# Kernel tuning notes

Hardware: AMD Instinct MI355X
Metric: run time of the kernel (lower is better)

The kernel has to match this reference:

```python
import jax, jax.numpy as jnp
import numpy as np

N_HEAD = 16


def setup_inputs() -> dict:
    key = jax.random.key(0)
    k0, k1, k2, k3 = jax.random.split(key, 4)
    b, n, d = 4, 2048, 1024
    scale = d ** -0.5
    return {
        "x": jax.random.normal(k0, (b, n, d), jnp.float32),
        "Wk": jax.random.normal(k1, (d, d), jnp.float32) * scale,
        "Wq": jax.random.normal(k2, (d, d), jnp.float32) * scale,
        "Wv": jax.random.normal(k3, (d, d), jnp.float32) * scale,
    }


def reference(x, Wk, Wq, Wv):
    b, n, d = x.shape
    hd = d // N_HEAD
    # Linear layers: y = x @ W^T (torch nn.Linear convention), no bias.
    keys = (x @ Wk.T).reshape(b, n, N_HEAD, hd).transpose(0, 2, 1, 3)     # (b,h,n,hd)
    queries = (x @ Wq.T).reshape(b, n, N_HEAD, hd).transpose(0, 2, 1, 3)  # (b,h,n,hd)
    values = (x @ Wv.T).reshape(b, n, N_HEAD, hd).transpose(0, 2, 1, 3)   # computed but UNUSED, as in source
    del values
    # Source does: attn_scores = keys @ queries.transpose(-1,-2)
    # i.e. scores[b,h,i,j] = k_i . q_j ; softmax over j (query axis); no 1/sqrt(d) scaling.
    attn_scores = jnp.einsum("bhid,bhjd->bhij", keys, queries)
    weights = jax.nn.softmax(attn_scores, axis=-1)
    # Source does: weight_scores @ keys (keys, NOT values)
    weighted = jnp.einsum("bhij,bhjd->bhid", weights, keys)  # (b,h,n,hd)
    # Source reshapes (b,h,n,hd) directly to (b,n,h*hd) WITHOUT transposing back.
    return weighted.reshape(b, n, N_HEAD * hd)
```

## Files before the change

### kernel.cpp

```cpp
#include <hip/hip_runtime.h>
#include <cstdint>
#include <cstddef>

#define NTOK 2048
#define DMODEL 1024
#define HD 64
#define MROWS 8192

using f16x8  = __attribute__((ext_vector_type(8))) _Float16;
using f16x4  = __attribute__((ext_vector_type(4))) _Float16;
using f32x4  = __attribute__((ext_vector_type(4))) float;
using f32x16 = __attribute__((ext_vector_type(16))) float;
using u16x8  = __attribute__((ext_vector_type(8))) unsigned short;
using u32x4  = __attribute__((ext_vector_type(4))) unsigned int;

#define Z16 {0.f,0.f,0.f,0.f,0.f,0.f,0.f,0.f,0.f,0.f,0.f,0.f,0.f,0.f,0.f,0.f}

__device__ __forceinline__ unsigned pkf16(float a, float b) {
  return __builtin_bit_cast(unsigned, __builtin_amdgcn_cvt_pkrtz(a, b));
}
__device__ __forceinline__ void plswap(unsigned &a, unsigned &b) {
  auto r = __builtin_amdgcn_permlane32_swap(a, b, false, false);
  a = r[0]; b = r[1];
}
__device__ __forceinline__ float fexp2(float x) {
  return __builtin_amdgcn_exp2f(x);
}

__global__ __launch_bounds__(256) void cvt_f32_f16(const float* __restrict__ in,
                                                   _Float16* __restrict__ out,
                                                   int n4, float scale) {
  int idx = blockIdx.x * 256 + threadIdx.x;
  if (idx < n4) {
    float4 v = reinterpret_cast<const float4*>(in)[idx];
    f16x4 o;
    o.x = (_Float16)(v.x * scale); o.y = (_Float16)(v.y * scale);
    o.z = (_Float16)(v.z * scale); o.w = (_Float16)(v.w * scale);
    reinterpret_cast<f16x4*>(out)[idx] = o;
  }
}

__global__ __launch_bounds__(256) void cvt_w(const float* __restrict__ Wk,
                                             const float* __restrict__ Wq,
                                             _Float16* __restrict__ Wkb,
                                             _Float16* __restrict__ Wqb) {
  const int idx = blockIdx.x * 256 + threadIdx.x;
  const float* in = blockIdx.y ? Wq : Wk;
  _Float16* out = blockIdx.y ? Wqb : Wkb;
  const float scale = blockIdx.y ? 1.4426950408889634f : 1.0f;
  float4 v = reinterpret_cast<const float4*>(in)[idx];
  f16x4 o;
  o.x = (_Float16)(v.x * scale); o.y = (_Float16)(v.y * scale);
  o.z = (_Float16)(v.z * scale); o.w = (_Float16)(v.w * scale);
  reinterpret_cast<f16x4*>(out)[idx] = o;
}

#define GLDS16(g, l) __builtin_amdgcn_global_load_lds(                      \
    (const __attribute__((address_space(1))) void*)(g),                     \
    (__attribute__((address_space(3))) void*)(l), 16, 0, 0)

__global__ __launch_bounds__(256) void gemm_f16(
    const _Float16* __restrict__ X,
    const _Float16* __restrict__ Wk,
    const _Float16* __restrict__ Wq,
    _Float16* __restrict__ Kb,
    _Float16* __restrict__ Qb) {
  const _Float16* __restrict__ W = blockIdx.z ? Wq : Wk;
  _Float16* __restrict__ Y = blockIdx.z ? Qb : Kb;

  __shared__ _Float16 As[2][128 * 32];
  __shared__ _Float16 Bs[2][128 * 32];

  const int tid = threadIdx.x;
  const int lane = tid & 63;
  const int w = tid >> 6;
  const int m0 = blockIdx.x * 128;
  const int o0 = blockIdx.y * 128;

  const int srow = w * 32 + (lane >> 2);
  const int scol = (lane & 3) * 8;
  const _Float16* xsrc = X + (size_t)(m0 + srow) * DMODEL + scol;
  const _Float16* wsrc = W + (size_t)(o0 + srow) * DMODEL + scol;

  const int wr = w >> 1, wc = w & 1;
  const int arow = lane & 15, kg = lane >> 4;

  f32x4 zero = {0.f, 0.f, 0.f, 0.f};
  f32x4 acc[4][4];
#pragma unroll
  for (int mi = 0; mi < 4; ++mi)
#pragma unroll
    for (int ni = 0; ni < 4; ++ni) acc[mi][ni] = zero;

  GLDS16(xsrc,               &As[0][(w * 32) * 32]);
  GLDS16(xsrc + 16 * DMODEL, &As[0][(w * 32 + 16) * 32]);
  GLDS16(wsrc,               &Bs[0][(w * 32) * 32]);
  GLDS16(wsrc + 16 * DMODEL, &Bs[0][(w * 32 + 16) * 32]);

  for (int kt = 0; kt < 32; ++kt) {
    __syncthreads();
    if (kt + 1 < 32) {
      const int ko = (kt + 1) * 32;
      const int bn = (kt + 1) & 1;
      GLDS16(xsrc + ko,               &As[bn][(w * 32) * 32]);
      GLDS16(xsrc + ko + 16 * DMODEL, &As[bn][(w * 32 + 16) * 32]);
      GLDS16(wsrc + ko,               &Bs[bn][(w * 32) * 32]);
      GLDS16(wsrc + ko + 16 * DMODEL, &Bs[bn][(w * 32 + 16) * 32]);
    }
    const int buf = kt & 1;
    f16x8 af[4], bfr[4];
#pragma unroll
    for (int mi = 0; mi < 4; ++mi)
      af[mi] = *reinterpret_cast<const f16x8*>(
          &As[buf][(wr * 64 + mi * 16 + arow) * 32 + kg * 8]);
#pragma unroll
    for (int ni = 0; ni < 4; ++ni)
      bfr[ni] = *reinterpret_cast<const f16x8*>(
          &Bs[buf][(wc * 64 + ni * 16 + arow) * 32 + kg * 8]);
#pragma unroll
    for (int mi = 0; mi < 4; ++mi)
#pragma unroll
      for (int ni = 0; ni < 4; ++ni)
        acc[mi][ni] = __builtin_amdgcn_mfma_f32_16x16x32_f16(
            af[mi], bfr[ni], acc[mi][ni], 0, 0, 0);
  }

#pragma unroll
  for (int mi = 0; mi < 4; ++mi) {
#pragma unroll
    for (int ni = 0; ni < 4; ++ni) {
#pragma unroll
      for (int r = 0; r < 4; ++r) {
        const int m = m0 + wr * 64 + mi * 16 + kg * 4 + r;
        const int o = o0 + wc * 64 + ni * 16 + arow;
        Y[(size_t)m * DMODEL + o] = (_Float16)acc[mi][ni][r];
      }
    }
  }
}

__global__ __launch_bounds__(256) void pack_qkt(
    const _Float16* __restrict__ Qb,
    const _Float16* __restrict__ Kb,
    _Float16* __restrict__ Qp,
    _Float16* __restrict__ KTp) {
  const int blk = blockIdx.x;
  const int bh = blk >> 5;
  const int t64 = blk & 31;
  const int b = bh >> 4, h = bh & 15;
  const int tid = threadIdx.x;
  const _Float16* Src = blockIdx.y ? Kb : Qb;

  __shared__ _Float16 t[64][72];
#pragma unroll
  for (int rr = 0; rr < 2; ++rr) {
    const int c = tid + rr * 256;
    const int jr = c >> 3, dcol = (c & 7) * 8;
    *reinterpret_cast<f16x8*>(&t[jr][dcol]) =
        *reinterpret_cast<const f16x8*>(
            &Src[(size_t)(b * NTOK + t64 * 64 + jr) * DMODEL + h * HD + dcol]);
  }
  __syncthreads();
  if (blockIdx.y == 0) {
#pragma unroll
    for (int rr = 0; rr < 2; ++rr) {
      const int cI = tid + rr * 256;
      const int rs = cI >> 8, ks = (cI >> 6) & 3, l = cI & 63;
      f16x8 v = *reinterpret_cast<const f16x8*>(
          &t[rs * 32 + (l & 31)][ks * 16 + (l >> 5) * 8]);
      const size_t ch = ((size_t)(bh * 64 + t64 * 2 + rs) * 4 + ks) * 512 + l * 8;
      *reinterpret_cast<f16x8*>(&Qp[ch]) = v;
    }
  } else {
#pragma unroll
    for (int rr = 0; rr < 2; ++rr) {
      const int cI = tid + rr * 256;
      const int ds = cI >> 8, ks = (cI >> 6) & 3, l = cI & 63;
      const int col = ds * 32 + (l & 31);
      const int row0 = ks * 16 + (l >> 5) * 8;
      f16x8 v;
#pragma unroll
      for (int e = 0; e < 8; ++e) v[e] = t[row0 + e][col];
      const size_t ch = (((size_t)(bh * 32 + t64) * 2 + ds) * 4 + ks) * 512 + l * 8;
      *reinterpret_cast<f16x8*>(&KTp[ch]) = v;
    }
  }
}

__global__ __launch_bounds__(256) void attn_mfma(
    const _Float16* __restrict__ Kb,
    const _Float16* __restrict__ Qp,
    const _Float16* __restrict__ KTp,
    float* __restrict__ out) {
  const int bid = blockIdx.x;
  const int myid = (bid & 7) * 128 + (bid >> 3);
  const int bh = myid >> 4;
  const int itile = myid & 15;
  const int b = bh >> 4, h = bh & 15;
  const int tid = threadIdx.x, lane = tid & 63, w = tid >> 6;
  const int l31 = lane & 31;
  const int hi = lane >> 5;
  const int hi8 = hi * 8;
  const int i0 = itile * 128 + w * 32;

  const _Float16* Kh    = Kb + (size_t)b * NTOK * DMODEL + h * HD;
  const _Float16* qsrc  = Qp  + (size_t)bh * 131072 + lane * 8;
  const _Float16* ktsrc = KTp + (size_t)bh * 131072 + lane * 8;

  __shared__ _Float16 QL[2][8][512];
  __shared__ _Float16 KL[2][8][512];
  __shared__ float lsl[4][32];
  __shared__ float scl[4][32];

  f16x8 kbf[4];
#pragma unroll
  for (int ks = 0; ks < 4; ++ks)
    kbf[ks] = *reinterpret_cast<const f16x8*>(
        &Kh[(size_t)(i0 + l31) * DMODEL + ks * 16 + hi8]);

  const f32x16 z16v = Z16;
  f32x16 o0 = z16v, o1 = z16v;
  float mreg = -1e30f, ls = 0.f;

  {
    const int c0 = w * 2, c1 = w * 2 + 1;
    GLDS16(qsrc  + (size_t)c0 * 512, &QL[0][c0][0]);
    GLDS16(qsrc  + (size_t)c1 * 512, &QL[0][c1][0]);
    GLDS16(ktsrc + (size_t)c0 * 512, &KL[0][c0][0]);
    GLDS16(ktsrc + (size_t)c1 * 512, &KL[0][c1][0]);
  }

  for (int jt = 0; jt < 32; ++jt) {
    const int buf = jt & 1;
    __syncthreads();
    if (jt + 1 < 32) {
      const int nb = buf ^ 1;
      const size_t tb = (size_t)(jt + 1) * 8 * 512;
      const int c0 = w * 2, c1 = w * 2 + 1;
      GLDS16(qsrc  + tb + (size_t)c0 * 512, &QL[nb][c0][0]);
      GLDS16(qsrc  + tb + (size_t)c1 * 512, &QL[nb][c1][0]);
      GLDS16(ktsrc + tb + (size_t)c0 * 512, &KL[nb][c0][0]);
      GLDS16(ktsrc + tb + (size_t)c1 * 512, &KL[nb][c1][0]);
    }

    f16x8 q0[4], q1[4];
#pragma unroll
    for (int ks = 0; ks < 4; ++ks) {
      q0[ks] = *reinterpret_cast<const f16x8*>(&QL[buf][ks][lane * 8]);
      q1[ks] = *reinterpret_cast<const f16x8*>(&QL[buf][4 + ks][lane * 8]);
    }

    f32x16 s0 = z16v, s1 = z16v;
    __builtin_amdgcn_s_setprio(1);
#pragma unroll
    for (int ks = 0; ks < 4; ++ks) {
      s0 = __builtin_amdgcn_mfma_f32_32x32x16_f16(q0[ks], kbf[ks], s0, 0, 0, 0);
      s1 = __builtin_amdgcn_mfma_f32_32x32x16_f16(q1[ks], kbf[ks], s1, 0, 0, 0);
    }
    __builtin_amdgcn_s_setprio(0);

    f16x8 kt0[4], kt1[4];
#pragma unroll
    for (int ks = 0; ks < 4; ++ks) {
      kt0[ks] = *reinterpret_cast<const f16x8*>(&KL[buf][ks][lane * 8]);
      kt1[ks] = *reinterpret_cast<const f16x8*>(&KL[buf][4 + ks][lane * 8]);
    }

    float m0 = fmaxf(s0[0], s1[0]);
    float m1 = fmaxf(s0[1], s1[1]);
    float m2 = fmaxf(s0[2], s1[2]);
    float m3 = fmaxf(s0[3], s1[3]);
#pragma unroll
    for (int r = 4; r < 16; r += 4) {
      m0 = fmaxf(m0, fmaxf(s0[r], s1[r]));
      m1 = fmaxf(m1, fmaxf(s0[r + 1], s1[r + 1]));
      m2 = fmaxf(m2, fmaxf(s0[r + 2], s1[r + 2]));
      m3 = fmaxf(m3, fmaxf(s0[r + 3], s1[r + 3]));
    }
    float pm = fmaxf(fmaxf(m0, m1), fmaxf(m2, m3));
    pm = fmaxf(pm, __shfl_xor(pm, 32));

    if (!__all(pm <= mreg + 8.0f)) {
      const float mn = fmaxf(mreg, pm);
      const float sc = fexp2(mreg - mn);
      ls *= sc;
      mreg = mn;
      scl[w][l31] = sc;
#pragma unroll
      for (int r = 0; r < 16; ++r) {
        const int il = (r & 3) + 8 * (r >> 2) + 4 * hi;
        const float scr = scl[w][il];
        o0[r] *= scr; o1[r] *= scr;
      }
    }

    float p0a[16], p1a[16];
#pragma unroll
    for (int r = 0; r < 16; ++r) {
      p0a[r] = fexp2(s0[r] - mreg);
      p1a[r] = fexp2(s1[r] - mreg);
    }
    float l0 = 0.f, l1 = 0.f, l2 = 0.f, l3 = 0.f;
#pragma unroll
    for (int r = 0; r < 16; r += 4) {
      l0 += p0a[r]     + p1a[r];
      l1 += p0a[r + 1] + p1a[r + 1];
      l2 += p0a[r + 2] + p1a[r + 2];
      l3 += p0a[r + 3] + p1a[r + 3];
    }
    ls += (l0 + l1) + (l2 + l3);

    f16x8 pfr[4];
    {
      unsigned a0 = pkf16(p0a[0], p0a[1]),  b0 = pkf16(p0a[4], p0a[5]);
      unsigned a1 = pkf16(p0a[2], p0a[3]),  b1 = pkf16(p0a[6], p0a[7]);
      plswap(a0, b0); plswap(a1, b1);
      u32x4 t; t[0] = a0; t[1] = a1; t[2] = b0; t[3] = b1;
      pfr[0] = __builtin_bit_cast(f16x8, t);
      unsigned a2 = pkf16(p0a[8], p0a[9]),   b2 = pkf16(p0a[12], p0a[13]);
      unsigned a3 = pkf16(p0a[10], p0a[11]), b3 = pkf16(p0a[14], p0a[15]);
      plswap(a2, b2); plswap(a3, b3);
      t[0] = a2; t[1] = a3; t[2] = b2; t[3] = b3;
      pfr[1] = __builtin_bit_cast(f16x8, t);
      unsigned a4 = pkf16(p1a[0], p1a[1]),  b4 = pkf16(p1a[4], p1a[5]);
      unsigned a5 = pkf16(p1a[2], p1a[3]),  b5 = pkf16(p1a[6], p1a[7]);
      plswap(a4, b4); plswap(a5, b5);
      t[0] = a4; t[1] = a5; t[2] = b4; t[3] = b5;
      pfr[2] = __builtin_bit_cast(f16x8, t);
      unsigned a6 = pkf16(p1a[8], p1a[9]),   b6 = pkf16(p1a[12], p1a[13]);
      unsigned a7 = pkf16(p1a[10], p1a[11]), b7 = pkf16(p1a[14], p1a[15]);
      plswap(a6, b6); plswap(a7, b7);
      t[0] = a6; t[1] = a7; t[2] = b6; t[3] = b7;
      pfr[3] = __builtin_bit_cast(f16x8, t);
    }

    __builtin_amdgcn_s_setprio(1);
#pragma unroll
    for (int ks = 0; ks < 4; ++ks) {
      o0 = __builtin_amdgcn_mfma_f32_32x32x16_f16(pfr[ks], kt0[ks], o0, 0, 0, 0);
      o1 = __builtin_amdgcn_mfma_f32_32x32x16_f16(pfr[ks], kt1[ks], o1, 0, 0, 0);
    }
    __builtin_amdgcn_s_setprio(0);
  }

  lsl[w][l31] = ls + __shfl_xor(ls, 32);
  __syncthreads();
#pragma unroll
  for (int r = 0; r < 16; ++r) {
    const int il = (r & 3) + 8 * (r >> 2) + 4 * hi;
    const float inv = 1.0f / lsl[w][il];
    const size_t rowb = ((size_t)bh * NTOK + i0 + il) * HD;
    out[rowb + l31]      = o0[r] * inv;
    out[rowb + 32 + l31] = o1[r] * inv;
  }
}

extern "C" void kernel_launch(void* const* d_in, const int* in_sizes, int n_in,
                              void* d_out, int out_size, void* d_ws, size_t ws_size,
                              hipStream_t stream) {
  const float* x  = (const float*)d_in[0];
  const float* Wk = (const float*)d_in[1];
  const float* Wq = (const float*)d_in[2];
  float* out = (float*)d_out;

  _Float16* xb  = (_Float16*)d_ws;
  _Float16* Qp  = xb;
  _Float16* Wkb = xb + (size_t)8388608;
  _Float16* Wqb = Wkb + (size_t)1048576;
  _Float16* Kb  = Wqb + (size_t)1048576;
  _Float16* Qb  = Kb + (size_t)8388608;
  _Float16* KTp = Qb;

  cvt_f32_f16<<<8192, 256, 0, stream>>>(x, xb, 2097152, 1.0f);
  cvt_w<<<dim3(1024, 2), 256, 0, stream>>>(Wk, Wq, Wkb, Wqb);

  dim3 ggrid(MROWS / 128, DMODEL / 128, 2);
  gemm_f16<<<ggrid, 256, 0, stream>>>(xb, Wkb, Wqb, Kb, Qb);

  pack_qkt<<<dim3(2048, 2), 256, 0, stream>>>(Qb, Kb, Qp, KTp);

  attn_mfma<<<1024, 256, 0, stream>>>(Kb, Qp, KTp, out);
}
```

Before: 189.4 us.

## Drop LDS staging in attention; load Q/KT fragments directly from global with smaller key tiles

```diff
diff --git a/kernel.cpp b/kernel.cpp
--- a/kernel.cpp
+++ b/kernel.cpp
@@ -187,7 +187,7 @@
   }
 }
 
-__global__ __launch_bounds__(256) void attn_mfma(
+__global__ __launch_bounds__(256, 3) void attn_mfma(
     const _Float16* __restrict__ Kb,
     const _Float16* __restrict__ Qp,
     const _Float16* __restrict__ KTp,
@@ -203,12 +203,10 @@
   const int hi8 = hi * 8;
   const int i0 = itile * 128 + w * 32;
 
-  const _Float16* Kh    = Kb + (size_t)b * NTOK * DMODEL + h * HD;
-  const _Float16* qsrc  = Qp  + (size_t)bh * 131072 + lane * 8;
-  const _Float16* ktsrc = KTp + (size_t)bh * 131072 + lane * 8;
-
-  __shared__ _Float16 QL[2][8][512];
-  __shared__ _Float16 KL[2][8][512];
+  const _Float16* Kh   = Kb + (size_t)b * NTOK * DMODEL + h * HD;
+  const _Float16* qpp  = Qp  + (size_t)bh * 131072 + lane * 8;
+  const _Float16* ktpp = KTp + (size_t)bh * 131072 + lane * 8;
+
   __shared__ float lsl[4][32];
   __shared__ float scl[4][32];
 
@@ -222,60 +220,39 @@
   f32x16 o0 = z16v, o1 = z16v;
   float mreg = -1e30f, ls = 0.f;
 
-  {
-    const int c0 = w * 2, c1 = w * 2 + 1;
-    GLDS16(qsrc  + (size_t)c0 * 512, &QL[0][c0][0]);
-    GLDS16(qsrc  + (size_t)c1 * 512, &QL[0][c1][0]);
-    GLDS16(ktsrc + (size_t)c0 * 512, &KL[0][c0][0]);
-    GLDS16(ktsrc + (size_t)c1 * 512, &KL[0][c1][0]);
-  }
-
-  for (int jt = 0; jt < 32; ++jt) {
-    const int buf = jt & 1;
-    __syncthreads();
-    if (jt + 1 < 32) {
-      const int nb = buf ^ 1;
-      const size_t tb = (size_t)(jt + 1) * 8 * 512;
-      const int c0 = w * 2, c1 = w * 2 + 1;
-      GLDS16(qsrc  + tb + (size_t)c0 * 512, &QL[nb][c0][0]);
-      GLDS16(qsrc  + tb + (size_t)c1 * 512, &QL[nb][c1][0]);
-      GLDS16(ktsrc + tb + (size_t)c0 * 512, &KL[nb][c0][0]);
-      GLDS16(ktsrc + tb + (size_t)c1 * 512, &KL[nb][c1][0]);
-    }
-
-    f16x8 q0[4], q1[4];
-#pragma unroll
-    for (int ks = 0; ks < 4; ++ks) {
-      q0[ks] = *reinterpret_cast<const f16x8*>(&QL[buf][ks][lane * 8]);
-      q1[ks] = *reinterpret_cast<const f16x8*>(&QL[buf][4 + ks][lane * 8]);
-    }
-
-    f32x16 s0 = z16v, s1 = z16v;
+  for (int jt = 0; jt < 64; ++jt) {
+    f16x8 q[4];
+#pragma unroll
+    for (int ks = 0; ks < 4; ++ks)
+      q[ks] = *reinterpret_cast<const f16x8*>(qpp + ((size_t)jt * 4 + ks) * 512);
+
+    f32x16 s = z16v;
     __builtin_amdgcn_s_setprio(1);
 #pragma unroll
-    for (int ks = 0; ks < 4; ++ks) {
-      s0 = __builtin_amdgcn_mfma_f32_32x32x16_f16(q0[ks], kbf[ks], s0, 0, 0, 0);
-      s1 = __builtin_amdgcn_mfma_f32_32x32x16_f16(q1[ks], kbf[ks], s1, 0, 0, 0);
-    }
+    for (int ks = 0; ks < 4; ++ks)
+      s = __builtin_amdgcn_mfma_f32_32x32x16_f16(q[ks], kbf[ks], s, 0, 0, 0);
     __builtin_amdgcn_s_setprio(0);
 
-    f16x8 kt0[4], kt1[4];
-#pragma unroll
-    for (int ks = 0; ks < 4; ++ks) {
-      kt0[ks] = *reinterpret_cast<const f16x8*>(&KL[buf][ks][lane * 8]);
-      kt1[ks] = *reinterpret_cast<const f16x8*>(&KL[buf][4 + ks][lane * 8]);
-    }
-
-    float m0 = fmaxf(s0[0], s1[0]);
-    float m1 = fmaxf(s0[1], s1[1]);
-    float m2 = fmaxf(s0[2], s1[2]);
-    float m3 = fmaxf(s0[3], s1[3]);
-#pragma unroll
-    for (int r = 4; r < 16; r += 4) {
-      m0 = fmaxf(m0, fmaxf(s0[r], s1[r]));
-      m1 = fmaxf(m1, fmaxf(s0[r + 1], s1[r + 1]));
-      m2 = fmaxf(m2, fmaxf(s0[r + 2], s1[r + 2]));
-      m3 = fmaxf(m3, fmaxf(s0[r + 3], s1[r + 3]));
+    f16x8 kt0[2], kt1[2];
+    {
+      const size_t base = ((size_t)(jt >> 1) * 8 + (size_t)(jt & 1) * 2) * 512;
+#pragma unroll
+      for (int kk = 0; kk < 2; ++kk) {
+        kt0[kk] = *reinterpret_cast<const f16x8*>(ktpp + base + (size_t)kk * 512);
+        kt1[kk] = *reinterpret_cast<const f16x8*>(ktpp + base + (size_t)(4 + kk) * 512);
+      }
+    }
+
+    float m0 = fmaxf(s[0], s[4]);
+    float m1 = fmaxf(s[1], s[5]);
+    float m2 = fmaxf(s[2], s[6]);
+    float m3 = fmaxf(s[3], s[7]);
+#pragma unroll
+    for (int r = 8; r < 16; r += 4) {
+      m0 = fmaxf(m0, s[r]);
+      m1 = fmaxf(m1, s[r + 1]);
+      m2 = fmaxf(m2, s[r + 2]);
+      m3 = fmaxf(m3, s[r + 3]);
     }
     float pm = fmaxf(fmaxf(m0, m1), fmaxf(m2, m3));
     pm = fmaxf(pm, __shfl_xor(pm, 32));
@@ -294,51 +271,35 @@
       }
     }
 
-    float p0a[16], p1a[16];
-#pragma unroll
-    for (int r = 0; r < 16; ++r) {
-      p0a[r] = fexp2(s0[r] - mreg);
-      p1a[r] = fexp2(s1[r] - mreg);
-    }
-    float l0 = 0.f, l1 = 0.f, l2 = 0.f, l3 = 0.f;
-#pragma unroll
-    for (int r = 0; r < 16; r += 4) {
-      l0 += p0a[r]     + p1a[r];
-      l1 += p0a[r + 1] + p1a[r + 1];
-      l2 += p0a[r + 2] + p1a[r + 2];
-      l3 += p0a[r + 3] + p1a[r + 3];
-    }
-    ls += (l0 + l1) + (l2 + l3);
-
-    f16x8 pfr[4];
+#pragma unroll
+    for (int r = 0; r < 16; ++r) s[r] = fexp2(s[r] - mreg);
     {
-      unsigned a0 = pkf16(p0a[0], p0a[1]),  b0 = pkf16(p0a[4], p0a[5]);
-      unsigned a1 = pkf16(p0a[2], p0a[3]),  b1 = pkf16(p0a[6], p0a[7]);
+      float l0 = (s[0] + s[4]) + (s[8] + s[12]);
+      float l1 = (s[1] + s[5]) + (s[9] + s[13]);
+      float l2 = (s[2] + s[6]) + (s[10] + s[14]);
+      float l3 = (s[3] + s[7]) + (s[11] + s[15]);
+      ls += (l0 + l1) + (l2 + l3);
+    }
+
+    f16x8 pfr[2];
+    {
+      unsigned a0 = pkf16(s[0], s[1]),  b0 = pkf16(s[4], s[5]);
+      unsigned a1 = pkf16(s[2], s[3]),  b1 = pkf16(s[6], s[7]);
       plswap(a0, b0); plswap(a1, b1);
       u32x4 t; t[0] = a0; t[1] = a1; t[2] = b0; t[3] = b1;
       pfr[0] = __builtin_bit_cast(f16x8, t);
-      unsigned a2 = pkf16(p0a[8], p0a[9]),   b2 = pkf16(p0a[12], p0a[13]);
-      unsigned a3 = pkf16(p0a[10], p0a[11]), b3 = pkf16(p0a[14], p0a[15]);
+      unsigned a2 = pkf16(s[8], s[9]),   b2 = pkf16(s[12], s[13]);
+      unsigned a3 = pkf16(s[10], s[11]), b3 = pkf16(s[14], s[15]);
       plswap(a2, b2); plswap(a3, b3);
       t[0] = a2; t[1] = a3; t[2] = b2; t[3] = b3;
       pfr[1] = __builtin_bit_cast(f16x8, t);
-      unsigned a4 = pkf16(p1a[0], p1a[1]),  b4 = pkf16(p1a[4], p1a[5]);
-      unsigned a5 = pkf16(p1a[2], p1a[3]),  b5 = pkf16(p1a[6], p1a[7]);
-      plswap(a4, b4); plswap(a5, b5);
-      t[0] = a4; t[1] = a5; t[2] = b4; t[3] = b5;
-      pfr[2] = __builtin_bit_cast(f16x8, t);
-      unsigned a6 = pkf16(p1a[8], p1a[9]),   b6 = pkf16(p1a[12], p1a[13]);
-      unsigned a7 = pkf16(p1a[10], p1a[11]), b7 = pkf16(p1a[14], p1a[15]);
-      plswap(a6, b6); plswap(a7, b7);
-      t[0] = a6; t[1] = a7; t[2] = b6; t[3] = b7;
-      pfr[3] = __builtin_bit_cast(f16x8, t);
     }
 
     __builtin_amdgcn_s_setprio(1);
 #pragma unroll
-    for (int ks = 0; ks < 4; ++ks) {
-      o0 = __builtin_amdgcn_mfma_f32_32x32x16_f16(pfr[ks], kt0[ks], o0, 0, 0, 0);
-      o1 = __builtin_amdgcn_mfma_f32_32x32x16_f16(pfr[ks], kt1[ks], o1, 0, 0, 0);
+    for (int kk = 0; kk < 2; ++kk) {
+      o0 = __builtin_amdgcn_mfma_f32_32x32x16_f16(pfr[kk], kt0[kk], o0, 0, 0, 0);
+      o1 = __builtin_amdgcn_mfma_f32_32x32x16_f16(pfr[kk], kt1[kk], o1, 0, 0, 0);
     }
     __builtin_amdgcn_s_setprio(0);
   }
```

Result: faster. 184.4 us (-2.7%).
